# Performance work log

Hardware: AMD Instinct MI355X
Metric: run time of the kernel (lower is better)

Reference implementation:

```python
import jax, jax.numpy as jnp
import numpy as np

N = 100000
E = 1600000
D_IN = 128
D_H = 128


def setup_inputs() -> dict:
    key = jax.random.key(0)
    ks = jax.random.split(key, 8)
    x = jax.random.normal(ks[0], (N, D_IN), dtype=jnp.float32)
    edge_index = jax.random.randint(ks[1], (2, E), 0, N, dtype=jnp.int64)
    # Glorot-ish init for weights, zeros for biases (PyG GCNConv default: glorot W, zero bias)
    W1 = jax.random.normal(ks[2], (D_IN, D_H), dtype=jnp.float32) / np.sqrt(D_IN)
    b1 = jnp.zeros((D_H,), dtype=jnp.float32)
    W2 = jax.random.normal(ks[3], (D_H, D_H), dtype=jnp.float32) / np.sqrt(D_H)
    b2 = jnp.zeros((D_H,), dtype=jnp.float32)
    Wout = jax.random.normal(ks[4], (D_H, 1), dtype=jnp.float32) / np.sqrt(D_H)
    bout = jnp.zeros((1,), dtype=jnp.float32)
    return {"x": x, "edge_index": edge_index, "W1": W1, "b1": b1,
            "W2": W2, "b2": b2, "Wout": Wout, "bout": bout}


def _gcn_conv(x, W, b, src, dst, inv_sqrt_deg, inv_deg):
    # PyG GCNConv: h = x @ W; out = sum_{j in N(i)} norm_ij * h_j + (1/deg_i) * h_i + b
    # norm_ij = deg_i^-1/2 * deg_j^-1/2 with self-loops folded into deg.
    h = x @ W                                   # [N, D]
    norm = inv_sqrt_deg[src] * inv_sqrt_deg[dst]  # [E]
    msgs = h[src] * norm[:, None]               # [E, D] gather
    agg = jax.ops.segment_sum(msgs, dst, num_segments=x.shape[0])  # [N, D] scatter
    agg = agg + h * inv_deg[:, None]            # self-loop term (norm = 1/deg)
    return agg + b


def reference(x, edge_index, W1, b1, W2, b2, Wout, bout):
    src = edge_index[0]
    dst = edge_index[1]
    n = x.shape[0]
    # degree with self-loops: deg_i = 1 + #incoming edges to i
    deg = 1.0 + jax.ops.segment_sum(jnp.ones((src.shape[0],), dtype=x.dtype), dst, num_segments=n)
    inv_sqrt_deg = jax.lax.rsqrt(deg)
    inv_deg = 1.0 / deg
    h = jax.nn.relu(_gcn_conv(x, W1, b1, src, dst, inv_sqrt_deg, inv_deg))
    h = jax.nn.relu(_gcn_conv(h, W2, b2, src, dst, inv_sqrt_deg, inv_deg))
    logits = h @ Wout + bout                    # [N, 1]
    return jax.nn.sigmoid(logits).squeeze(-1)   # [N]
```

## Files before the change

kernel.cpp:

```cpp
#include <hip/hip_runtime.h>
#include <cstddef>

#define CAPD 64
#define BSZ 512
#define BSH 9
#define CHUNK 8192
#define BCAP 12288

typedef unsigned int uint;
typedef unsigned short ushort;
typedef unsigned char uchar;
typedef float f32x4 __attribute__((ext_vector_type(4)));
typedef _Float16 f16x8 __attribute__((ext_vector_type(8)));

__device__ inline float h_lo(uint v) {
    union { ushort u; _Float16 h; } c; c.u = (ushort)(v & 0xFFFFu); return (float)c.h;
}
__device__ inline float h_hi(uint v) {
    union { ushort u; _Float16 h; } c; c.u = (ushort)(v >> 16); return (float)c.h;
}
__device__ inline ushort h_bits(float x) {
    union { _Float16 h; ushort u; } c; c.h = (_Float16)x; return c.u;
}
__device__ inline uint h_pack(float a, float b) {
    return (uint)h_bits(a) | ((uint)h_bits(b) << 16);
}
__device__ inline float ub0(uint v) { return (float)(v & 0xFFu); }
__device__ inline float ub1(uint v) { return (float)((v >> 8) & 0xFFu); }
__device__ inline float ub2(uint v) { return (float)((v >> 16) & 0xFFu); }
__device__ inline float ub3(uint v) { return (float)(v >> 24); }

__global__ __launch_bounds__(256) void prep_kernel(int* __restrict__ bucketCursor, int nb,
                                                   const float* __restrict__ W1,
                                                   const float* __restrict__ W2,
                                                   uint* __restrict__ Wt1,
                                                   uint* __restrict__ Wt2) {
    __shared__ float ws[128][129];
    int bid = blockIdx.x, tid = threadIdx.x;
    if (bid == 0) {
        for (int i = tid; i < nb; i += 256) bucketCursor[i] = 0;
        return;
    }
    const float* W = (bid == 2) ? W2 : W1;
    uint* O = (bid == 2) ? Wt2 : Wt1;
#pragma unroll
    for (int j = 0; j < 16; ++j) {
        int q = tid + 256 * j;
        int k = q >> 5, c = (q & 31) * 4;
        float4 v = *reinterpret_cast<const float4*>(W + k * 128 + c);
        ws[k][c] = v.x; ws[k][c + 1] = v.y; ws[k][c + 2] = v.z; ws[k][c + 3] = v.w;
    }
    __syncthreads();
#pragma unroll
    for (int j = 0; j < 32; ++j) {
        int q = tid + 256 * j;
        int ncol = q >> 6, kw = q & 63;
        O[q] = h_pack(ws[2 * kw][ncol], ws[2 * kw + 1][ncol]);
    }
}

__device__ __forceinline__ void gemm_core(const void* __restrict__ A, int aF16,
                                          const uint* __restrict__ Wt,
                                          const float* __restrict__ scale,
                                          uint* __restrict__ Tq,
                                          float* __restrict__ Ts,
                                          int n, int m0, int tid, uint* SH) {
    char* shb = (char*)SH;
    if (aF16) {
        const uint* Af = (const uint*)A;
#pragma unroll
        for (int j = 0; j < 8; ++j) {
            int q = tid + 256 * j;
            int row = q >> 4, c16 = q & 15;
            int grow = m0 + row;
            uint4 v = make_uint4(0u, 0u, 0u, 0u);
            if (grow < n) v = *reinterpret_cast<const uint4*>(Af + (size_t)grow * 64 + c16 * 4);
            *reinterpret_cast<uint4*>(shb + row * 256 + ((c16 * 16) ^ ((row & 7) << 4))) = v;
        }
    } else {
        const float* Af = (const float*)A;
#pragma unroll
        for (int j = 0; j < 8; ++j) {
            int q = tid + 256 * j;
            int row = q >> 4, c16 = q & 15;
            int grow = m0 + row;
            uint4 o = make_uint4(0u, 0u, 0u, 0u);
            if (grow < n) {
                float4 v0 = *reinterpret_cast<const float4*>(Af + (size_t)grow * 128 + c16 * 8);
                float4 v1 = *reinterpret_cast<const float4*>(Af + (size_t)grow * 128 + c16 * 8 + 4);
                o.x = h_pack(v0.x, v0.y); o.y = h_pack(v0.z, v0.w);
                o.z = h_pack(v1.x, v1.y); o.w = h_pack(v1.z, v1.w);
            }
            *reinterpret_cast<uint4*>(shb + row * 256 + ((c16 * 16) ^ ((row & 7) << 4))) = o;
        }
    }
#pragma unroll
    for (int j = 0; j < 8; ++j) {
        int q = tid + 256 * j;
        int col = q >> 4, c16 = q & 15;
        uint4 v = *reinterpret_cast<const uint4*>(Wt + col * 64 + c16 * 4);
        *reinterpret_cast<uint4*>(shb + 32768 + col * 256 + ((c16 * 16) ^ ((col & 7) << 4))) = v;
    }
    __syncthreads();

    const int w = tid >> 6, l = tid & 63;
    const int lrow = l & 15, kg = l >> 4;
    const int swz = (lrow & 7) << 4;

    f32x4 acc[2][8] = {};
#pragma unroll
    for (int kk = 0; kk < 4; ++kk) {
        const int koff = (kk * 64 + kg * 16) ^ swz;
        f16x8 a[2], b[8];
#pragma unroll
        for (int mr = 0; mr < 2; ++mr) {
            int r = w * 32 + mr * 16 + lrow;
            a[mr] = *reinterpret_cast<const f16x8*>(shb + r * 256 + koff);
        }
#pragma unroll
        for (int nc = 0; nc < 8; ++nc) {
            int c = nc * 16 + lrow;
            b[nc] = *reinterpret_cast<const f16x8*>(shb + 32768 + c * 256 + koff);
        }
#pragma unroll
        for (int mr = 0; mr < 2; ++mr)
#pragma unroll
            for (int nc = 0; nc < 8; ++nc)
                acc[mr][nc] = __builtin_amdgcn_mfma_f32_16x16x32_f16(a[mr], b[nc], acc[mr][nc], 0, 0, 0);
    }
    __syncthreads();

    ushort* Cs = (ushort*)SH;
#pragma unroll
    for (int mr = 0; mr < 2; ++mr) {
        int rb = w * 32 + mr * 16 + kg * 4;
#pragma unroll
        for (int i = 0; i < 4; ++i) {
            int grow = m0 + rb + i;
            float s = scale ? ((grow < n) ? scale[grow] : 0.f) : 1.f;
#pragma unroll
            for (int nc = 0; nc < 8; ++nc)
                Cs[(rb + i) * 136 + nc * 16 + lrow] = h_bits(s * acc[mr][nc][i]);
        }
    }
    __syncthreads();
    const uint* Cw = (const uint*)SH;
#pragma unroll
    for (int j = 0; j < 8; ++j) {
        int q = tid + 256 * j;
        int row = q >> 4, c8 = q & 15;
        int grow = m0 + row;
        uint4 v = *reinterpret_cast<const uint4*>(Cw + row * 68 + c8 * 4);
        float f0 = h_lo(v.x), f1 = h_hi(v.x), f2 = h_lo(v.y), f3 = h_hi(v.y);
        float f4 = h_lo(v.z), f5 = h_hi(v.z), f6 = h_lo(v.w), f7 = h_hi(v.w);
        float mx = fmaxf(fmaxf(fmaxf(fabsf(f0), fabsf(f1)), fmaxf(fabsf(f2), fabsf(f3))),
                         fmaxf(fmaxf(fabsf(f4), fabsf(f5)), fmaxf(fabsf(f6), fabsf(f7))));
#pragma unroll
        for (int off = 8; off > 0; off >>= 1) mx = fmaxf(mx, __shfl_xor(mx, off, 16));
        mx = fmaxf(mx, 1e-20f);
        float inv = 127.f / mx;
        int q0 = (int)rintf(f0 * inv) + 128, q1 = (int)rintf(f1 * inv) + 128;
        int q2 = (int)rintf(f2 * inv) + 128, q3 = (int)rintf(f3 * inv) + 128;
        int q4 = (int)rintf(f4 * inv) + 128, q5 = (int)rintf(f5 * inv) + 128;
        int q6 = (int)rintf(f6 * inv) + 128, q7 = (int)rintf(f7 * inv) + 128;
        uint w0 = (uint)q0 | ((uint)q1 << 8) | ((uint)q2 << 16) | ((uint)q3 << 24);
        uint w1 = (uint)q4 | ((uint)q5 << 8) | ((uint)q6 << 16) | ((uint)q7 << 24);
        if (grow < n) {
            *reinterpret_cast<uint2*>(Tq + (size_t)grow * 32 + c8 * 2) = make_uint2(w0, w1);
            if (c8 == 0) Ts[grow] = mx * (1.f / 127.f);
        }
    }
}

__global__ __launch_bounds__(256) void p3gemm1(const int* __restrict__ esrc,
                                               const int* __restrict__ edst, int E,
                                               int nb, int NB2,
                                               int* __restrict__ bucketCursor,
                                               unsigned* __restrict__ gSorted,
                                               const float* __restrict__ x,
                                               const uint* __restrict__ Wt1,
                                               uint* __restrict__ Tq,
                                               float* __restrict__ Ts, int N) {
    __shared__ __align__(16) char SHB[78848];
    int bid = blockIdx.x, tid = threadIdx.x;
    if (bid >= NB2) {
        gemm_core(x, 0, Wt1, nullptr, Tq, Ts, N, (bid - NB2) * 128, tid, (uint*)SHB);
        return;
    }
    uint*  payL = (uint*)SHB;
    uint*  outL = (uint*)(SHB + 32768);
    uchar* bktL = (uchar*)(SHB + 65536);
    int*   hist   = (int*)(SHB + 73728);
    int*   segoff = hist + 256;
    int*   cursor = segoff + 256;
    int*   gbase  = cursor + 256;
    int*   sc     = gbase + 256;
    int e0 = bid * CHUNK;
    int m = min(E - e0, CHUNK);
    for (int i = tid; i < m; i += 256) {
        unsigned d = (unsigned)edst[e0 + i];
        unsigned s = (unsigned)esrc[e0 + i];
        payL[i] = s | ((d & (BSZ - 1)) << 23);
        bktL[i] = (uchar)(d >> BSH);
    }
    hist[tid] = 0;
    __syncthreads();
    for (int i = tid; i < m; i += 256)
        atomicAdd(&hist[bktL[i]], 1);
    __syncthreads();
    sc[tid] = hist[tid];
    __syncthreads();
    for (int off = 1; off < 256; off <<= 1) {
        int v = (tid >= off) ? sc[tid - off] : 0;
        __syncthreads();
        sc[tid] += v;
        __syncthreads();
    }
    segoff[tid] = sc[tid] - hist[tid];
    cursor[tid] = segoff[tid];
    if (tid < nb && hist[tid] > 0) gbase[tid] = atomicAdd(&bucketCursor[tid], hist[tid]);
    __syncthreads();
    for (int i = tid; i < m; i += 256) {
        int b = (int)bktL[i];
        int p = atomicAdd(&cursor[b], 1);
        outL[p] = payL[i];
    }
    __syncthreads();
    int wave = tid >> 6, lane = tid & 63;
    for (int b = wave; b < nb; b += 4) {
        int off = segoff[b], len = hist[b];
        if (len == 0) continue;
        int gb = gbase[b];
        unsigned* dst = gSorted + (size_t)b * BCAP;
        for (int i = lane; i < len; i += 64)
            if (gb + i < BCAP) dst[gb + i] = outL[off + i];
    }
}

__global__ __launch_bounds__(256) void p4_build(const unsigned* __restrict__ gSorted,
                                                const int* __restrict__ bucketCursor,
                                                int nb, int N, int* __restrict__ cnt,
                                                float* __restrict__ isd,
                                                int* __restrict__ ell,
                                                const float* __restrict__ Ts,
                                                float* __restrict__ Tsc) {
    __shared__ unsigned ellL[128 * CAPD];
    __shared__ int cntL[128];
    int bid = blockIdx.x, tid = threadIdx.x;
    int bucket = bid >> 2;
    unsigned sub = (unsigned)(bid & 3);
    int n0 = bid * 128;
    int nValid = min(128, N - n0);
    if (nValid <= 0) return;
    for (int i = tid; i < 128; i += 256) cntL[i] = 0;
    __syncthreads();
    int len = bucketCursor[bucket];
    if (len > BCAP) len = BCAP;
    const unsigned* seg = gSorted + (size_t)bucket * BCAP;
    for (int i = tid; i < len; i += 256) {
        unsigned e = seg[i];
        unsigned dl = e >> 23;
        if ((dl >> 7) == sub) {
            int r = (int)(dl & 127u);
            int p = atomicAdd(&cntL[r], 1);
            if (p < CAPD) ellL[r * CAPD + p] = e & 0x7FFFFFu;
        }
    }
    __syncthreads();
    int total = nValid * CAPD;
    const int* ellLi = (const int*)ellL;
    for (int i = tid; i < total; i += 256) {
        int row = i >> 6, pos = i & 63;
        int c = cntL[row];
        if (pos < min(c, CAPD))
            ell[(size_t)n0 * CAPD + i] = ellLi[i];
    }
    for (int i = tid; i < nValid; i += 256) {
        int c = cntL[i];
        float iv = rsqrtf(1.0f + (float)c);
        cnt[n0 + i] = c;
        isd[n0 + i] = iv;
        Tsc[n0 + i] = Ts[n0 + i] * iv;
    }
}

__global__ __launch_bounds__(256) void gemm2_kernel(const uint* __restrict__ Hb,
                                                    const uint* __restrict__ Wt,
                                                    const float* __restrict__ isd,
                                                    uint* __restrict__ Tq,
                                                    float* __restrict__ Ts, int n) {
    __shared__ __align__(16) uint SH[16384];
    gemm_core(Hb, 1, Wt, isd, Tq, Ts, n, blockIdx.x * 128, threadIdx.x, SH);
}

__global__ __launch_bounds__(256) void agg_kernel(const uint* __restrict__ Tq,
                                                  const float* __restrict__ Tsc,
                                                  const int* __restrict__ ell,
                                                  const int* __restrict__ cnt,
                                                  const float* __restrict__ isd,
                                                  const float* __restrict__ bias,
                                                  uint* __restrict__ Hb, int n) {
    int node = (int)((blockIdx.x * 256 + threadIdx.x) >> 4);
    int ln = threadIdx.x & 15;
    if (node >= n) return;
    const uint2* T2 = (const uint2*)Tq;
    float di = isd[node];
    int c = cnt[node];
    if (c > CAPD) c = CAPD;
    const int* row = ell + (size_t)node * CAPD;
    float a0, a1, a2, a3, a4, a5, a6, a7, ssum;
    {
        uint2 v = T2[(size_t)node * 16 + ln];
        float sc = Tsc[node];
        ssum = sc;
        a0 = sc * ub0(v.x); a1 = sc * ub1(v.x); a2 = sc * ub2(v.x); a3 = sc * ub3(v.x);
        a4 = sc * ub0(v.y); a5 = sc * ub1(v.y); a6 = sc * ub2(v.y); a7 = sc * ub3(v.y);
    }
    int j = 0;
    for (; j + 8 <= c; j += 8) {
        int4 sa = *reinterpret_cast<const int4*>(row + j);
        int4 sb = *reinterpret_cast<const int4*>(row + j + 4);
        uint2 v0 = T2[(size_t)sa.x * 16 + ln]; float c0 = Tsc[sa.x];
        uint2 v1 = T2[(size_t)sa.y * 16 + ln]; float c1 = Tsc[sa.y];
        uint2 v2 = T2[(size_t)sa.z * 16 + ln]; float c2 = Tsc[sa.z];
        uint2 v3 = T2[(size_t)sa.w * 16 + ln]; float c3 = Tsc[sa.w];
        uint2 v4 = T2[(size_t)sb.x * 16 + ln]; float c4 = Tsc[sb.x];
        uint2 v5 = T2[(size_t)sb.y * 16 + ln]; float c5 = Tsc[sb.y];
        uint2 v6 = T2[(size_t)sb.z * 16 + ln]; float c6 = Tsc[sb.z];
        uint2 v7 = T2[(size_t)sb.w * 16 + ln]; float c7 = Tsc[sb.w];
        ssum += ((c0 + c1) + (c2 + c3)) + ((c4 + c5) + (c6 + c7));
        a0 = fmaf(c0, ub0(v0.x), fmaf(c1, ub0(v1.x), fmaf(c2, ub0(v2.x), fmaf(c3, ub0(v3.x),
             fmaf(c4, ub0(v4.x), fmaf(c5, ub0(v5.x), fmaf(c6, ub0(v6.x), fmaf(c7, ub0(v7.x), a0))))))));
        a1 = fmaf(c0, ub1(v0.x), fmaf(c1, ub1(v1.x), fmaf(c2, ub1(v2.x), fmaf(c3, ub1(v3.x),
             fmaf(c4, ub1(v4.x), fmaf(c5, ub1(v5.x), fmaf(c6, ub1(v6.x), fmaf(c7, ub1(v7.x), a1))))))));
        a2 = fmaf(c0, ub2(v0.x), fmaf(c1, ub2(v1.x), fmaf(c2, ub2(v2.x), fmaf(c3, ub2(v3.x),
             fmaf(c4, ub2(v4.x), fmaf(c5, ub2(v5.x), fmaf(c6, ub2(v6.x), fmaf(c7, ub2(v7.x), a2))))))));
        a3 = fmaf(c0, ub3(v0.x), fmaf(c1, ub3(v1.x), fmaf(c2, ub3(v2.x), fmaf(c3, ub3(v3.x),
             fmaf(c4, ub3(v4.x), fmaf(c5, ub3(v5.x), fmaf(c6, ub3(v6.x), fmaf(c7, ub3(v7.x), a3))))))));
        a4 = fmaf(c0, ub0(v0.y), fmaf(c1, ub0(v1.y), fmaf(c2, ub0(v2.y), fmaf(c3, ub0(v3.y),
             fmaf(c4, ub0(v4.y), fmaf(c5, ub0(v5.y), fmaf(c6, ub0(v6.y), fmaf(c7, ub0(v7.y), a4))))))));
        a5 = fmaf(c0, ub1(v0.y), fmaf(c1, ub1(v1.y), fmaf(c2, ub1(v2.y), fmaf(c3, ub1(v3.y),
             fmaf(c4, ub1(v4.y), fmaf(c5, ub1(v5.y), fmaf(c6, ub1(v6.y), fmaf(c7, ub1(v7.y), a5))))))));
        a6 = fmaf(c0, ub2(v0.y), fmaf(c1, ub2(v1.y), fmaf(c2, ub2(v2.y), fmaf(c3, ub2(v3.y),
             fmaf(c4, ub2(v4.y), fmaf(c5, ub2(v5.y), fmaf(c6, ub2(v6.y), fmaf(c7, ub2(v7.y), a6))))))));
        a7 = fmaf(c0, ub3(v0.y), fmaf(c1, ub3(v1.y), fmaf(c2, ub3(v2.y), fmaf(c3, ub3(v3.y),
             fmaf(c4, ub3(v4.y), fmaf(c5, ub3(v5.y), fmaf(c6, ub3(v6.y), fmaf(c7, ub3(v7.y), a7))))))));
    }
    for (; j + 4 <= c; j += 4) {
        int4 s4 = *reinterpret_cast<const int4*>(row + j);
        uint2 v0 = T2[(size_t)s4.x * 16 + ln]; float c0 = Tsc[s4.x];
        uint2 v1 = T2[(size_t)s4.y * 16 + ln]; float c1 = Tsc[s4.y];
        uint2 v2 = T2[(size_t)s4.z * 16 + ln]; float c2 = Tsc[s4.z];
        uint2 v3 = T2[(size_t)s4.w * 16 + ln]; float c3 = Tsc[s4.w];
        ssum += (c0 + c1) + (c2 + c3);
        a0 = fmaf(c0, ub0(v0.x), fmaf(c1, ub0(v1.x), fmaf(c2, ub0(v2.x), fmaf(c3, ub0(v3.x), a0))));
        a1 = fmaf(c0, ub1(v0.x), fmaf(c1, ub1(v1.x), fmaf(c2, ub1(v2.x), fmaf(c3, ub1(v3.x), a1))));
        a2 = fmaf(c0, ub2(v0.x), fmaf(c1, ub2(v1.x), fmaf(c2, ub2(v2.x), fmaf(c3, ub2(v3.x), a2))));
        a3 = fmaf(c0, ub3(v0.x), fmaf(c1, ub3(v1.x), fmaf(c2, ub3(v2.x), fmaf(c3, ub3(v3.x), a3))));
        a4 = fmaf(c0, ub0(v0.y), fmaf(c1, ub0(v1.y), fmaf(c2, ub0(v2.y), fmaf(c3, ub0(v3.y), a4))));
        a5 = fmaf(c0, ub1(v0.y), fmaf(c1, ub1(v1.y), fmaf(c2, ub1(v2.y), fmaf(c3, ub1(v3.y), a5))));
        a6 = fmaf(c0, ub2(v0.y), fmaf(c1, ub2(v1.y), fmaf(c2, ub2(v2.y), fmaf(c3, ub2(v3.y), a6))));
        a7 = fmaf(c0, ub3(v0.y), fmaf(c1, ub3(v1.y), fmaf(c2, ub3(v2.y), fmaf(c3, ub3(v3.y), a7))));
    }
    for (; j < c; ++j) {
        int s = row[j];
        uint2 v = T2[(size_t)s * 16 + ln];
        float sc = Tsc[s];
        ssum += sc;
        a0 = fmaf(sc, ub0(v.x), a0); a1 = fmaf(sc, ub1(v.x), a1);
        a2 = fmaf(sc, ub2(v.x), a2); a3 = fmaf(sc, ub3(v.x), a3);
        a4 = fmaf(sc, ub0(v.y), a4); a5 = fmaf(sc, ub1(v.y), a5);
        a6 = fmaf(sc, ub2(v.y), a6); a7 = fmaf(sc, ub3(v.y), a7);
    }
    float off = 128.f * ssum;
    float4 bv0 = *reinterpret_cast<const float4*>(bias + ln * 8);
    float4 bv1 = *reinterpret_cast<const float4*>(bias + ln * 8 + 4);
    float h0 = fmaxf(fmaf(di, a0 - off, bv0.x), 0.f);
    float h1 = fmaxf(fmaf(di, a1 - off, bv0.y), 0.f);
    float h2 = fmaxf(fmaf(di, a2 - off, bv0.z), 0.f);
    float h3 = fmaxf(fmaf(di, a3 - off, bv0.w), 0.f);
    float h4 = fmaxf(fmaf(di, a4 - off, bv1.x), 0.f);
    float h5 = fmaxf(fmaf(di, a5 - off, bv1.y), 0.f);
    float h6 = fmaxf(fmaf(di, a6 - off, bv1.z), 0.f);
    float h7 = fmaxf(fmaf(di, a7 - off, bv1.w), 0.f);
    uint4 o;
    o.x = h_pack(h0, h1); o.y = h_pack(h2, h3);
    o.z = h_pack(h4, h5); o.w = h_pack(h6, h7);
    *reinterpret_cast<uint4*>(Hb + (size_t)node * 64 + ln * 4) = o;
}

__global__ __launch_bounds__(256) void agg_out_kernel(const uint* __restrict__ Tq,
                                                      const float* __restrict__ Ts,
                                                      const int* __restrict__ ell,
                                                      const int* __restrict__ cnt,
                                                      const float* __restrict__ isd,
                                                      const float* __restrict__ bias,
                                                      const float* __restrict__ Wout,
                                                      const float* __restrict__ bout,
                                                      float* __restrict__ out, int n) {
    int node = (int)((blockIdx.x * 256 + threadIdx.x) >> 4);
    int ln = threadIdx.x & 15;
    if (node >= n) return;
    const uint2* T2 = (const uint2*)Tq;
    float di = isd[node];
    int c = cnt[node];
    if (c > CAPD) c = CAPD;
    const int* row = ell + (size_t)node * CAPD;
    float a0, a1, a2, a3, a4, a5, a6, a7, ssum;
    {
        uint2 v = T2[(size_t)node * 16 + ln];
        float sc = Ts[node];
        ssum = sc;
        a0 = sc * ub0(v.x); a1 = sc * ub1(v.x); a2 = sc * ub2(v.x); a3 = sc * ub3(v.x);
        a4 = sc * ub0(v.y); a5 = sc * ub1(v.y); a6 = sc * ub2(v.y); a7 = sc * ub3(v.y);
    }
    int j = 0;
    for (; j + 8 <= c; j += 8) {
        int4 sa = *reinterpret_cast<const int4*>(row + j);
        int4 sb = *reinterpret_cast<const int4*>(row + j + 4);
        uint2 v0 = T2[(size_t)sa.x * 16 + ln]; float c0 = Ts[sa.x];
        uint2 v1 = T2[(size_t)sa.y * 16 + ln]; float c1 = Ts[sa.y];
        uint2 v2 = T2[(size_t)sa.z * 16 + ln]; float c2 = Ts[sa.z];
        uint2 v3 = T2[(size_t)sa.w * 16 + ln]; float c3 = Ts[sa.w];
        uint2 v4 = T2[(size_t)sb.x * 16 + ln]; float c4 = Ts[sb.x];
        uint2 v5 = T2[(size_t)sb.y * 16 + ln]; float c5 = Ts[sb.y];
        uint2 v6 = T2[(size_t)sb.z * 16 + ln]; float c6 = Ts[sb.z];
        uint2 v7 = T2[(size_t)sb.w * 16 + ln]; float c7 = Ts[sb.w];
        ssum += ((c0 + c1) + (c2 + c3)) + ((c4 + c5) + (c6 + c7));
        a0 = fmaf(c0, ub0(v0.x), fmaf(c1, ub0(v1.x), fmaf(c2, ub0(v2.x), fmaf(c3, ub0(v3.x),
             fmaf(c4, ub0(v4.x), fmaf(c5, ub0(v5.x), fmaf(c6, ub0(v6.x), fmaf(c7, ub0(v7.x), a0))))))));
        a1 = fmaf(c0, ub1(v0.x), fmaf(c1, ub1(v1.x), fmaf(c2, ub1(v2.x), fmaf(c3, ub1(v3.x),
             fmaf(c4, ub1(v4.x), fmaf(c5, ub1(v5.x), fmaf(c6, ub1(v6.x), fmaf(c7, ub1(v7.x), a1))))))));
        a2 = fmaf(c0, ub2(v0.x), fmaf(c1, ub2(v1.x), fmaf(c2, ub2(v2.x), fmaf(c3, ub2(v3.x),
             fmaf(c4, ub2(v4.x), fmaf(c5, ub2(v5.x), fmaf(c6, ub2(v6.x), fmaf(c7, ub2(v7.x), a2))))))));
        a3 = fmaf(c0, ub3(v0.x), fmaf(c1, ub3(v1.x), fmaf(c2, ub3(v2.x), fmaf(c3, ub3(v3.x),
             fmaf(c4, ub3(v4.x), fmaf(c5, ub3(v5.x), fmaf(c6, ub3(v6.x), fmaf(c7, ub3(v7.x), a3))))))));
        a4 = fmaf(c0, ub0(v0.y), fmaf(c1, ub0(v1.y), fmaf(c2, ub0(v2.y), fmaf(c3, ub0(v3.y),
             fmaf(c4, ub0(v4.y), fmaf(c5, ub0(v5.y), fmaf(c6, ub0(v6.y), fmaf(c7, ub0(v7.y), a4))))))));
        a5 = fmaf(c0, ub1(v0.y), fmaf(c1, ub1(v1.y), fmaf(c2, ub1(v2.y), fmaf(c3, ub1(v3.y),
             fmaf(c4, ub1(v4.y), fmaf(c5, ub1(v5.y), fmaf(c6, ub1(v6.y), fmaf(c7, ub1(v7.y), a5))))))));
        a6 = fmaf(c0, ub2(v0.y), fmaf(c1, ub2(v1.y), fmaf(c2, ub2(v2.y), fmaf(c3, ub2(v3.y),
             fmaf(c4, ub2(v4.y), fmaf(c5, ub2(v5.y), fmaf(c6, ub2(v6.y), fmaf(c7, ub2(v7.y), a6))))))));
        a7 = fmaf(c0, ub3(v0.y), fmaf(c1, ub3(v1.y), fmaf(c2, ub3(v2.y), fmaf(c3, ub3(v3.y),
             fmaf(c4, ub3(v4.y), fmaf(c5, ub3(v5.y), fmaf(c6, ub3(v6.y), fmaf(c7, ub3(v7.y), a7))))))));
    }
    for (; j + 4 <= c; j += 4) {
        int4 s4 = *reinterpret_cast<const int4*>(row + j);
        uint2 v0 = T2[(size_t)s4.x * 16 + ln]; float c0 = Ts[s4.x];
        uint2 v1 = T2[(size_t)s4.y * 16 + ln]; float c1 = Ts[s4.y];
        uint2 v2 = T2[(size_t)s4.z * 16 + ln]; float c2 = Ts[s4.z];
        uint2 v3 = T2[(size_t)s4.w * 16 + ln]; float c3 = Ts[s4.w];
        ssum += (c0 + c1) + (c2 + c3);
        a0 = fmaf(c0, ub0(v0.x), fmaf(c1, ub0(v1.x), fmaf(c2, ub0(v2.x), fmaf(c3, ub0(v3.x), a0))));
        a1 = fmaf(c0, ub1(v0.x), fmaf(c1, ub1(v1.x), fmaf(c2, ub1(v2.x), fmaf(c3, ub1(v3.x), a1))));
        a2 = fmaf(c0, ub2(v0.x), fmaf(c1, ub2(v1.x), fmaf(c2, ub2(v2.x), fmaf(c3, ub2(v3.x), a2))));
        a3 = fmaf(c0, ub3(v0.x), fmaf(c1, ub3(v1.x), fmaf(c2, ub3(v2.x), fmaf(c3, ub3(v3.x), a3))));
        a4 = fmaf(c0, ub0(v0.y), fmaf(c1, ub0(v1.y), fmaf(c2, ub0(v2.y), fmaf(c3, ub0(v3.y), a4))));
        a5 = fmaf(c0, ub1(v0.y), fmaf(c1, ub1(v1.y), fmaf(c2, ub1(v2.y), fmaf(c3, ub1(v3.y), a5))));
        a6 = fmaf(c0, ub2(v0.y), fmaf(c1, ub2(v1.y), fmaf(c2, ub2(v2.y), fmaf(c3, ub2(v3.y), a6))));
        a7 = fmaf(c0, ub3(v0.y), fmaf(c1, ub3(v1.y), fmaf(c2, ub3(v2.y), fmaf(c3, ub3(v3.y), a7))));
    }
    for (; j < c; ++j) {
        int s = row[j];
        uint2 v = T2[(size_t)s * 16 + ln];
        float sc = Ts[s];
        ssum += sc;
        a0 = fmaf(sc, ub0(v.x), a0); a1 = fmaf(sc, ub1(v.x), a1);
        a2 = fmaf(sc, ub2(v.x), a2); a3 = fmaf(sc, ub3(v.x), a3);
        a4 = fmaf(sc, ub0(v.y), a4); a5 = fmaf(sc, ub1(v.y), a5);
        a6 = fmaf(sc, ub2(v.y), a6); a7 = fmaf(sc, ub3(v.y), a7);
    }
    float off = 128.f * ssum;
    float4 bv0 = *reinterpret_cast<const float4*>(bias + ln * 8);
    float4 bv1 = *reinterpret_cast<const float4*>(bias + ln * 8 + 4);
    float4 wv0 = *reinterpret_cast<const float4*>(Wout + ln * 8);
    float4 wv1 = *reinterpret_cast<const float4*>(Wout + ln * 8 + 4);
    float h0 = fmaxf(fmaf(di, a0 - off, bv0.x), 0.f);
    float h1 = fmaxf(fmaf(di, a1 - off, bv0.y), 0.f);
    float h2 = fmaxf(fmaf(di, a2 - off, bv0.z), 0.f);
    float h3 = fmaxf(fmaf(di, a3 - off, bv0.w), 0.f);
    float h4 = fmaxf(fmaf(di, a4 - off, bv1.x), 0.f);
    float h5 = fmaxf(fmaf(di, a5 - off, bv1.y), 0.f);
    float h6 = fmaxf(fmaf(di, a6 - off, bv1.z), 0.f);
    float h7 = fmaxf(fmaf(di, a7 - off, bv1.w), 0.f);
    float v = fmaf(h0, wv0.x, fmaf(h1, wv0.y, fmaf(h2, wv0.z, fmaf(h3, wv0.w,
              fmaf(h4, wv1.x, fmaf(h5, wv1.y, fmaf(h6, wv1.z, h7 * wv1.w)))))));
#pragma unroll
    for (int off2 = 8; off2 > 0; off2 >>= 1) v += __shfl_xor(v, off2, 16);
    if (ln == 0) out[node] = 1.f / (1.f + expf(-(v + bout[0])));
}

extern "C" void kernel_launch(void* const* d_in, const int* in_sizes, int n_in,
                              void* d_out, int out_size, void* d_ws, size_t ws_size,
                              hipStream_t stream) {
    const float* x    = (const float*)d_in[0];
    const int*   ei   = (const int*)d_in[1];
    const float* W1   = (const float*)d_in[2];
    const float* b1   = (const float*)d_in[3];
    const float* W2   = (const float*)d_in[4];
    const float* b2   = (const float*)d_in[5];
    const float* Wout = (const float*)d_in[6];
    const float* bout = (const float*)d_in[7];
    float* out = (float*)d_out;

    const int N = in_sizes[0] / 128;
    const int E = in_sizes[1] / 2;
    const int* esrc = ei;
    const int* edst = ei + E;

    char* p = (char*)d_ws;
    auto alloc = [&](size_t bytes) {
        char* r = p;
        p += (bytes + 255) & ~(size_t)255;
        return (void*)r;
    };
    const int nb  = (N + BSZ - 1) / BSZ;
    const int NB2 = (E + CHUNK - 1) / CHUNK;

    int*   cnt = (int*)  alloc((size_t)N * 4);
    float* isd = (float*)alloc((size_t)N * 4);
    int*   ell = (int*)  alloc((size_t)N * CAPD * 4);
    uint*  Tq  = (uint*) alloc((size_t)N * 32 * 4);
    float* Ts  = (float*)alloc((size_t)(N + 4) * 4);
    float* Tsc = (float*)alloc((size_t)(N + 4) * 4);
    uint*  Hb  = (uint*) alloc((size_t)N * 64 * 4);
    uint*  Wt1 = (uint*) alloc(8192 * 4);
    uint*  Wt2 = (uint*) alloc(8192 * 4);
    unsigned* gSorted      = (unsigned*)alloc((size_t)nb * BCAP * 4);
    int*      bucketCursor = (int*)     alloc((size_t)nb * 4);

    const int gblocks = (N + 127) / 128;
    const int ablocks = (N + 15) / 16;

    prep_kernel<<<3, 256, 0, stream>>>(bucketCursor, nb, W1, W2, Wt1, Wt2);
    p3gemm1<<<NB2 + gblocks, 256, 0, stream>>>(esrc, edst, E, nb, NB2, bucketCursor,
                                               gSorted, x, Wt1, Tq, Ts, N);
    p4_build<<<4 * nb, 256, 0, stream>>>(gSorted, bucketCursor, nb, N, cnt, isd, ell, Ts, Tsc);
    agg_kernel<<<ablocks, 256, 0, stream>>>(Tq, Tsc, ell, cnt, isd, b1, Hb, N);
    gemm2_kernel<<<gblocks, 256, 0, stream>>>(Hb, Wt2, isd, Tq, Ts, N);
    agg_out_kernel<<<ablocks, 256, 0, stream>>>(Tq, Ts, ell, cnt, isd, b2, Wout, bout, out, N);
}
```

Baseline: 156.3 us.

## Load GEMM operands directly from global memory and shrink LDS footprint

The GEMM core now feeds MFMA operands straight from global memory (A rows and transposed weights) instead of staging them through swizzled shared memory, dropping one barrier and the staging copies. The edge-bucketing kernel no longer keeps a payload buffer in LDS; it re-reads src/dst from global memory when scattering, which cuts the LDS allocation from about 77KB to about 45KB. The aim is higher occupancy for the fused sort/GEMM kernel and gemm2, at the cost of redundant, less coalesced global loads (each weight row is read by every wave) and a second pass over the edge arrays.

```diff
diff --git a/kernel.cpp b/kernel.cpp
--- a/kernel.cpp
+++ b/kernel.cpp
@@ -12,6 +12,8 @@
 typedef unsigned char uchar;
 typedef float f32x4 __attribute__((ext_vector_type(4)));
 typedef _Float16 f16x8 __attribute__((ext_vector_type(8)));
+
+union U4H8 { uint4 u; f16x8 h; };
 
 __device__ inline float h_lo(uint v) {
     union { ushort u; _Float16 h; } c; c.u = (ushort)(v & 0xFFFFu); return (float)c.h;
@@ -64,63 +66,41 @@
                                           const float* __restrict__ scale,
                                           uint* __restrict__ Tq,
                                           float* __restrict__ Ts,
-                                          int n, int m0, int tid, uint* SH) {
-    char* shb = (char*)SH;
-    if (aF16) {
-        const uint* Af = (const uint*)A;
-#pragma unroll
-        for (int j = 0; j < 8; ++j) {
-            int q = tid + 256 * j;
-            int row = q >> 4, c16 = q & 15;
-            int grow = m0 + row;
-            uint4 v = make_uint4(0u, 0u, 0u, 0u);
-            if (grow < n) v = *reinterpret_cast<const uint4*>(Af + (size_t)grow * 64 + c16 * 4);
-            *reinterpret_cast<uint4*>(shb + row * 256 + ((c16 * 16) ^ ((row & 7) << 4))) = v;
-        }
-    } else {
-        const float* Af = (const float*)A;
-#pragma unroll
-        for (int j = 0; j < 8; ++j) {
-            int q = tid + 256 * j;
-            int row = q >> 4, c16 = q & 15;
-            int grow = m0 + row;
-            uint4 o = make_uint4(0u, 0u, 0u, 0u);
-            if (grow < n) {
-                float4 v0 = *reinterpret_cast<const float4*>(Af + (size_t)grow * 128 + c16 * 8);
-                float4 v1 = *reinterpret_cast<const float4*>(Af + (size_t)grow * 128 + c16 * 8 + 4);
-                o.x = h_pack(v0.x, v0.y); o.y = h_pack(v0.z, v0.w);
-                o.z = h_pack(v1.x, v1.y); o.w = h_pack(v1.z, v1.w);
-            }
-            *reinterpret_cast<uint4*>(shb + row * 256 + ((c16 * 16) ^ ((row & 7) << 4))) = o;
-        }
-    }
-#pragma unroll
-    for (int j = 0; j < 8; ++j) {
-        int q = tid + 256 * j;
-        int col = q >> 4, c16 = q & 15;
-        uint4 v = *reinterpret_cast<const uint4*>(Wt + col * 64 + c16 * 4);
-        *reinterpret_cast<uint4*>(shb + 32768 + col * 256 + ((c16 * 16) ^ ((col & 7) << 4))) = v;
-    }
-    __syncthreads();
-
+                                          int n, int m0, int tid, ushort* SH) {
     const int w = tid >> 6, l = tid & 63;
     const int lrow = l & 15, kg = l >> 4;
-    const int swz = (lrow & 7) << 4;
 
     f32x4 acc[2][8] = {};
 #pragma unroll
     for (int kk = 0; kk < 4; ++kk) {
-        const int koff = (kk * 64 + kg * 16) ^ swz;
         f16x8 a[2], b[8];
 #pragma unroll
         for (int mr = 0; mr < 2; ++mr) {
-            int r = w * 32 + mr * 16 + lrow;
-            a[mr] = *reinterpret_cast<const f16x8*>(shb + r * 256 + koff);
+            int r = m0 + w * 32 + mr * 16 + lrow;
+            U4H8 t;
+            if (aF16) {
+                const uint* Af = (const uint*)A;
+                t.u = (r < n) ? *reinterpret_cast<const uint4*>(Af + (size_t)r * 64 + kk * 16 + kg * 4)
+                              : make_uint4(0u, 0u, 0u, 0u);
+            } else {
+                const float* Af = (const float*)A;
+                if (r < n) {
+                    float4 v0 = *reinterpret_cast<const float4*>(Af + (size_t)r * 128 + kk * 32 + kg * 8);
+                    float4 v1 = *reinterpret_cast<const float4*>(Af + (size_t)r * 128 + kk * 32 + kg * 8 + 4);
+                    t.u.x = h_pack(v0.x, v0.y); t.u.y = h_pack(v0.z, v0.w);
+                    t.u.z = h_pack(v1.x, v1.y); t.u.w = h_pack(v1.z, v1.w);
+                } else {
+                    t.u = make_uint4(0u, 0u, 0u, 0u);
+                }
+            }
+            a[mr] = t.h;
         }
 #pragma unroll
         for (int nc = 0; nc < 8; ++nc) {
             int c = nc * 16 + lrow;
-            b[nc] = *reinterpret_cast<const f16x8*>(shb + 32768 + c * 256 + koff);
+            U4H8 t;
+            t.u = *reinterpret_cast<const uint4*>(Wt + c * 64 + kk * 16 + kg * 4);
+            b[nc] = t.h;
         }
 #pragma unroll
         for (int mr = 0; mr < 2; ++mr)
@@ -128,9 +108,8 @@
             for (int nc = 0; nc < 8; ++nc)
                 acc[mr][nc] = __builtin_amdgcn_mfma_f32_16x16x32_f16(a[mr], b[nc], acc[mr][nc], 0, 0, 0);
     }
-    __syncthreads();
-
-    ushort* Cs = (ushort*)SH;
+
+    ushort* Cs = SH;
 #pragma unroll
     for (int mr = 0; mr < 2; ++mr) {
         int rb = w * 32 + mr * 16 + kg * 4;
@@ -181,32 +160,28 @@
                                                const uint* __restrict__ Wt1,
                                                uint* __restrict__ Tq,
                                                float* __restrict__ Ts, int N) {
-    __shared__ __align__(16) char SHB[78848];
+    __shared__ __align__(16) char SHB[46080];
     int bid = blockIdx.x, tid = threadIdx.x;
     if (bid >= NB2) {
-        gemm_core(x, 0, Wt1, nullptr, Tq, Ts, N, (bid - NB2) * 128, tid, (uint*)SHB);
+        gemm_core(x, 0, Wt1, nullptr, Tq, Ts, N, (bid - NB2) * 128, tid, (ushort*)SHB);
         return;
     }
-    uint*  payL = (uint*)SHB;
-    uint*  outL = (uint*)(SHB + 32768);
-    uchar* bktL = (uchar*)(SHB + 65536);
-    int*   hist   = (int*)(SHB + 73728);
+    uint*  outL = (uint*)SHB;
+    uchar* bktL = (uchar*)(SHB + 32768);
+    int*   hist   = (int*)(SHB + 40960);
     int*   segoff = hist + 256;
     int*   cursor = segoff + 256;
     int*   gbase  = cursor + 256;
     int*   sc     = gbase + 256;
     int e0 = bid * CHUNK;
     int m = min(E - e0, CHUNK);
+    hist[tid] = 0;
+    __syncthreads();
     for (int i = tid; i < m; i += 256) {
-        unsigned d = (unsigned)edst[e0 + i];
-        unsigned s = (unsigned)esrc[e0 + i];
-        payL[i] = s | ((d & (BSZ - 1)) << 23);
-        bktL[i] = (uchar)(d >> BSH);
-    }
-    hist[tid] = 0;
-    __syncthreads();
-    for (int i = tid; i < m; i += 256)
-        atomicAdd(&hist[bktL[i]], 1);
+        int b = edst[e0 + i] >> BSH;
+        bktL[i] = (uchar)b;
+        atomicAdd(&hist[b], 1);
+    }
     __syncthreads();
     sc[tid] = hist[tid];
     __syncthreads();
@@ -221,9 +196,11 @@
     if (tid < nb && hist[tid] > 0) gbase[tid] = atomicAdd(&bucketCursor[tid], hist[tid]);
     __syncthreads();
     for (int i = tid; i < m; i += 256) {
+        unsigned d = (unsigned)edst[e0 + i];
+        unsigned s = (unsigned)esrc[e0 + i];
         int b = (int)bktL[i];
         int p = atomicAdd(&cursor[b], 1);
-        outL[p] = payL[i];
+        outL[p] = s | ((d & (BSZ - 1)) << 23);
     }
     __syncthreads();
     int wave = tid >> 6, lane = tid & 63;
@@ -289,7 +266,7 @@
                                                     const float* __restrict__ isd,
                                                     uint* __restrict__ Tq,
                                                     float* __restrict__ Ts, int n) {
-    __shared__ __align__(16) uint SH[16384];
+    __shared__ __align__(16) ushort SH[128 * 136];
     gemm_core(Hb, 1, Wt, isd, Tq, Ts, n, blockIdx.x * 128, threadIdx.x, SH);
 }
 
```

Result: slower. 177.7 us (+13.7%).

## Halve GEMM tile rows and drop bucket payload staging to cut LDS usage

Applied to the files above, without the earlier changes.

The GEMM tile shrinks from 128 to 64 rows per block, with one 16-row MFMA strip per wave, which halves the accumulator registers and the A-tile LDS. The edge-bucketing path no longer stages packed payloads in LDS; it recomputes them by re-reading src/dst from global memory in the scatter pass, and the histogram is built in the first pass. Static LDS falls from about 77 KB to 48 KB, so more blocks can be resident per CU. The cost is twice as many GEMM blocks, weight tiles reloaded per block, and an extra global read of the edge arrays.

```diff
diff --git a/kernel.cpp b/kernel.cpp
--- a/kernel.cpp
+++ b/kernel.cpp
@@ -64,12 +64,11 @@
                                           const float* __restrict__ scale,
                                           uint* __restrict__ Tq,
                                           float* __restrict__ Ts,
-                                          int n, int m0, int tid, uint* SH) {
-    char* shb = (char*)SH;
+                                          int n, int m0, int tid, char* shb) {
     if (aF16) {
         const uint* Af = (const uint*)A;
 #pragma unroll
-        for (int j = 0; j < 8; ++j) {
+        for (int j = 0; j < 4; ++j) {
             int q = tid + 256 * j;
             int row = q >> 4, c16 = q & 15;
             int grow = m0 + row;
@@ -80,7 +79,7 @@
     } else {
         const float* Af = (const float*)A;
 #pragma unroll
-        for (int j = 0; j < 8; ++j) {
+        for (int j = 0; j < 4; ++j) {
             int q = tid + 256 * j;
             int row = q >> 4, c16 = q & 15;
             int grow = m0 + row;
@@ -99,7 +98,7 @@
         int q = tid + 256 * j;
         int col = q >> 4, c16 = q & 15;
         uint4 v = *reinterpret_cast<const uint4*>(Wt + col * 64 + c16 * 4);
-        *reinterpret_cast<uint4*>(shb + 32768 + col * 256 + ((c16 * 16) ^ ((col & 7) << 4))) = v;
+        *reinterpret_cast<uint4*>(shb + 16384 + col * 256 + ((c16 * 16) ^ ((col & 7) << 4))) = v;
     }
     __syncthreads();
 
@@ -107,46 +106,40 @@
     const int lrow = l & 15, kg = l >> 4;
     const int swz = (lrow & 7) << 4;
 
-    f32x4 acc[2][8] = {};
+    f32x4 acc[8] = {};
 #pragma unroll
     for (int kk = 0; kk < 4; ++kk) {
         const int koff = (kk * 64 + kg * 16) ^ swz;
-        f16x8 a[2], b[8];
-#pragma unroll
-        for (int mr = 0; mr < 2; ++mr) {
-            int r = w * 32 + mr * 16 + lrow;
-            a[mr] = *reinterpret_cast<const f16x8*>(shb + r * 256 + koff);
-        }
+        int r = w * 16 + lrow;
+        f16x8 a = *reinterpret_cast<const f16x8*>(shb + r * 256 + koff);
+        f16x8 b[8];
 #pragma unroll
         for (int nc = 0; nc < 8; ++nc) {
             int c = nc * 16 + lrow;
-            b[nc] = *reinterpret_cast<const f16x8*>(shb + 32768 + c * 256 + koff);
+            b[nc] = *reinterpret_cast<const f16x8*>(shb + 16384 + c * 256 + koff);
         }
 #pragma unroll
-        for (int mr = 0; mr < 2; ++mr)
-#pragma unroll
-            for (int nc = 0; nc < 8; ++nc)
-                acc[mr][nc] = __builtin_amdgcn_mfma_f32_16x16x32_f16(a[mr], b[nc], acc[mr][nc], 0, 0, 0);
-    }
-    __syncthreads();
-
-    ushort* Cs = (ushort*)SH;
-#pragma unroll
-    for (int mr = 0; mr < 2; ++mr) {
-        int rb = w * 32 + mr * 16 + kg * 4;
+        for (int nc = 0; nc < 8; ++nc)
+            acc[nc] = __builtin_amdgcn_mfma_f32_16x16x32_f16(a, b[nc], acc[nc], 0, 0, 0);
+    }
+    __syncthreads();
+
+    ushort* Cs = (ushort*)shb;
+    {
+        int rb = w * 16 + kg * 4;
 #pragma unroll
         for (int i = 0; i < 4; ++i) {
             int grow = m0 + rb + i;
             float s = scale ? ((grow < n) ? scale[grow] : 0.f) : 1.f;
 #pragma unroll
             for (int nc = 0; nc < 8; ++nc)
-                Cs[(rb + i) * 136 + nc * 16 + lrow] = h_bits(s * acc[mr][nc][i]);
+                Cs[(rb + i) * 136 + nc * 16 + lrow] = h_bits(s * acc[nc][i]);
         }
     }
     __syncthreads();
-    const uint* Cw = (const uint*)SH;
-#pragma unroll
-    for (int j = 0; j < 8; ++j) {
+    const uint* Cw = (const uint*)shb;
+#pragma unroll
+    for (int j = 0; j < 4; ++j) {
         int q = tid + 256 * j;
         int row = q >> 4, c8 = q & 15;
         int grow = m0 + row;
@@ -181,32 +174,28 @@
                                                const uint* __restrict__ Wt1,
                                                uint* __restrict__ Tq,
                                                float* __restrict__ Ts, int N) {
-    __shared__ __align__(16) char SHB[78848];
+    __shared__ __align__(16) char SHB[49152];
     int bid = blockIdx.x, tid = threadIdx.x;
     if (bid >= NB2) {
-        gemm_core(x, 0, Wt1, nullptr, Tq, Ts, N, (bid - NB2) * 128, tid, (uint*)SHB);
+        gemm_core(x, 0, Wt1, nullptr, Tq, Ts, N, (bid - NB2) * 64, tid, SHB);
         return;
     }
-    uint*  payL = (uint*)SHB;
-    uint*  outL = (uint*)(SHB + 32768);
-    uchar* bktL = (uchar*)(SHB + 65536);
-    int*   hist   = (int*)(SHB + 73728);
+    uint*  outL = (uint*)SHB;
+    uchar* bktL = (uchar*)(SHB + 32768);
+    int*   hist   = (int*)(SHB + 40960);
     int*   segoff = hist + 256;
     int*   cursor = segoff + 256;
     int*   gbase  = cursor + 256;
     int*   sc     = gbase + 256;
     int e0 = bid * CHUNK;
     int m = min(E - e0, CHUNK);
+    hist[tid] = 0;
+    __syncthreads();
     for (int i = tid; i < m; i += 256) {
-        unsigned d = (unsigned)edst[e0 + i];
-        unsigned s = (unsigned)esrc[e0 + i];
-        payL[i] = s | ((d & (BSZ - 1)) << 23);
-        bktL[i] = (uchar)(d >> BSH);
-    }
-    hist[tid] = 0;
-    __syncthreads();
-    for (int i = tid; i < m; i += 256)
-        atomicAdd(&hist[bktL[i]], 1);
+        int b = edst[e0 + i] >> BSH;
+        bktL[i] = (uchar)b;
+        atomicAdd(&hist[b], 1);
+    }
     __syncthreads();
     sc[tid] = hist[tid];
     __syncthreads();
@@ -221,9 +210,11 @@
     if (tid < nb && hist[tid] > 0) gbase[tid] = atomicAdd(&bucketCursor[tid], hist[tid]);
     __syncthreads();
     for (int i = tid; i < m; i += 256) {
+        unsigned d = (unsigned)edst[e0 + i];
+        unsigned s = (unsigned)esrc[e0 + i];
         int b = (int)bktL[i];
         int p = atomicAdd(&cursor[b], 1);
-        outL[p] = payL[i];
+        outL[p] = s | ((d & (BSZ - 1)) << 23);
     }
     __syncthreads();
     int wave = tid >> 6, lane = tid & 63;
@@ -289,8 +280,8 @@
                                                     const float* __restrict__ isd,
                                                     uint* __restrict__ Tq,
                                                     float* __restrict__ Ts, int n) {
-    __shared__ __align__(16) uint SH[16384];
-    gemm_core(Hb, 1, Wt, isd, Tq, Ts, n, blockIdx.x * 128, threadIdx.x, SH);
+    __shared__ __align__(16) char SHB[49152];
+    gemm_core(Hb, 1, Wt, isd, Tq, Ts, n, blockIdx.x * 64, threadIdx.x, SHB);
 }
 
 __global__ __launch_bounds__(256) void agg_kernel(const uint* __restrict__ Tq,
@@ -529,7 +520,7 @@
     unsigned* gSorted      = (unsigned*)alloc((size_t)nb * BCAP * 4);
     int*      bucketCursor = (int*)     alloc((size_t)nb * 4);
 
-    const int gblocks = (N + 127) / 128;
+    const int gblocks = (N + 63) / 64;
     const int ablocks = (N + 15) / 16;
 
     prep_kernel<<<3, 256, 0, stream>>>(bucketCursor, nb, W1, W2, Wt1, Wt2);
```

New measurement: 157.7 us. Within noise of the previous version (+0.9%).
